# Kernel optimization log

Hardware: AMD Instinct MI355X
Metric: run time of the kernel (lower is better)

## Reference

```python
import jax, jax.numpy as jnp
import numpy as np

B = 64        # number of graph segments
BASE = 384    # mean verts per segment
LMAX = 512    # pad length (counts in [256, 512])
H_DIM = 256
H_DIV = 128   # h_dim // h_dim_div
HEADS = 4
DH = H_DIV // HEADS  # 32


def _counts(seed):
    rng = np.random.default_rng(seed)
    d = rng.integers(-128, 129, B)
    d[1::2] = -d[::2]            # paired so the total is exactly B*BASE
    return (BASE + d).astype(np.int64)


def _pad_indices(counts, L):
    # Gather indices/mask mapping packed ragged tokens -> padded [B, L].
    counts = np.asarray(counts)
    off = np.concatenate([[0], np.cumsum(counts)[:-1]])
    ar = np.arange(L)[None, :]
    mask = ar < counts[:, None]
    idx = np.where(mask, off[:, None] + ar, 0)
    return idx, mask


def setup_inputs() -> dict:
    key = jax.random.key(0)
    ks = jax.random.split(key, 16)
    src_num_verts = _counts(0)
    dst_num_verts = _counts(1)
    total = B * BASE  # 24576 for both src and dst

    def w(k, shape):
        return 0.02 * jax.random.normal(k, shape, jnp.float32)

    return {
        'src_h': jax.random.normal(ks[0], (total, H_DIM), jnp.float32),
        'dst_h': jax.random.normal(ks[1], (total, H_DIM), jnp.float32),
        'src_num_verts': src_num_verts,
        'dst_num_verts': dst_num_verts,
        # 1x1 Conv1d == linear over channels
        'Wq': w(ks[2], (H_DIV, H_DIM)), 'bq': w(ks[3], (H_DIV,)),
        'Wk': w(ks[4], (H_DIV, H_DIM)), 'bk': w(ks[5], (H_DIV,)),
        'Wv': w(ks[6], (H_DIV, H_DIM)), 'bv': w(ks[7], (H_DIV,)),
        'Wm': w(ks[8], (H_DIV, H_DIV)), 'bm': w(ks[9], (H_DIV,)),
        'W1': w(ks[10], (H_DIM, H_DIM + H_DIV)), 'b1': w(ks[11], (H_DIM,)),
        'g1': 1.0 + 0.1 * jax.random.normal(ks[12], (H_DIM,), jnp.float32),
        'be1': w(ks[13], (H_DIM,)),
        'rm1': w(ks[14], (H_DIM,)),
        'rv1': jax.random.uniform(ks[15], (H_DIM,), jnp.float32, 0.5, 1.5),
        'W2': w(jax.random.fold_in(key, 100), (H_DIM, H_DIM)),
        'b2': w(jax.random.fold_in(key, 101), (H_DIM,)),
        'g2': 1.0 + 0.1 * jax.random.normal(jax.random.fold_in(key, 102), (H_DIM,), jnp.float32),
        'be2': w(jax.random.fold_in(key, 103), (H_DIM,)),
        'rm2': w(jax.random.fold_in(key, 104), (H_DIM,)),
        'rv2': jax.random.uniform(jax.random.fold_in(key, 105), (H_DIM,), jnp.float32, 0.5, 1.5),
    }


def _bn(x, g, b, rm, rv):
    # BatchNorm1d in eval mode (running stats)
    return (x - rm) / jnp.sqrt(rv + 1e-5) * g + b


def reference(src_h, dst_h, src_num_verts, dst_num_verts,
              Wq, bq, Wk, bk, Wv, bv, Wm, bm,
              W1, b1, g1, be1, rm1, rv1,
              W2, b2, g2, be2, rm2, rv2):
    didx, dmask = _pad_indices(dst_num_verts, LMAX)
    sidx, smask = _pad_indices(src_num_verts, LMAX)

    # fused projections over all packed tokens (1x1 conv == matmul)
    q = src_h_proj = dst_h @ Wq.T + bq        # [Nd, H_DIV]
    k = src_h @ Wk.T + bk                     # [Ns, H_DIV]
    v = src_h @ Wv.T + bv

    # pad to block-diagonal batched form; channel c = d*HEADS + h per torch view
    qp = q[didx].reshape(B, LMAX, DH, HEADS)
    kp = k[sidx].reshape(B, LMAX, DH, HEADS)
    vp = v[sidx].reshape(B, LMAX, DH, HEADS)

    scores = jnp.einsum('bndh,bmdh->bhnm', qp, kp) / (DH ** 0.5)
    scores = jnp.where(jnp.asarray(smask)[:, None, None, :], scores, -1e9)
    attn = jax.nn.softmax(scores, axis=-1)
    msg = jnp.einsum('bhnm,bmdh->bndh', attn, vp).reshape(B, LMAX, H_DIV)
    msg = msg @ Wm.T + bm                     # merge conv

    bb, ii = np.nonzero(dmask)                # unpad back to packed layout
    h_msg = msg[bb, ii]                       # [Nd, H_DIV]

    x = jnp.concatenate([dst_h, h_msg], axis=-1)
    x = _bn(x @ W1.T + b1, g1, be1, rm1, rv1)
    x = jax.nn.relu(x)
    x = _bn(x @ W2.T + b2, g2, be2, rm2, rv2)
    return dst_h + x
```

## Files before the change

### kernel.cpp

```cpp
#include <hip/hip_runtime.h>
#include <hip/hip_bf16.h>
#include <math.h>

#define B_SEG 64
#define HDIM 256
#define HDIV 128
#define NHEADS 4
#define DH 32
#define QSC 0.17677669529663687f

typedef unsigned short u16;
typedef unsigned int u32;

typedef __attribute__((ext_vector_type(8))) short s8v;
typedef __attribute__((ext_vector_type(4))) float f4v;

__device__ __forceinline__ u16 f2bf(float f) {
    u32 v;
    __builtin_memcpy(&v, &f, 4);
    u32 r = v + 0x7fffu + ((v >> 16) & 1u);
    return (u16)(r >> 16);
}

__device__ __forceinline__ void async_cp16(const u16* g, u16* l) {
    __builtin_amdgcn_global_load_lds(
        (const __attribute__((address_space(1))) u32*)g,
        (__attribute__((address_space(3))) u32*)l, 16, 0, 0);
}

__global__ __launch_bounds__(256) void k_prep(
    const float* __restrict__ Wq, const float* __restrict__ bq,
    const float* __restrict__ Wk, const float* __restrict__ bk,
    const float* __restrict__ Wv, const float* __restrict__ bv,
    const float* __restrict__ Wm, const float* __restrict__ bm,
    const float* __restrict__ W1, const float* __restrict__ b1,
    const float* __restrict__ g1, const float* __restrict__ be1,
    const float* __restrict__ rm1, const float* __restrict__ rv1,
    const float* __restrict__ W2, const float* __restrict__ b2,
    const float* __restrict__ g2, const float* __restrict__ be2,
    const float* __restrict__ rm2, const float* __restrict__ rv2,
    const int* __restrict__ sc_raw, const int* __restrict__ dc_raw,
    const float* __restrict__ src_h, const float* __restrict__ dst_h,
    int* __restrict__ meta,
    u16* __restrict__ pWq, u16* __restrict__ pWkv,
    u16* __restrict__ pW1f, u16* __restrict__ pW2,
    float* __restrict__ bqp, float* __restrict__ bkvp,
    float* __restrict__ sc1, float* __restrict__ sh1,
    float* __restrict__ sc2, float* __restrict__ sh2,
    u16* __restrict__ srcb, u16* __restrict__ dstb, int ntot) {
    if (blockIdx.x < 1028) {
        int idx = blockIdx.x * 256 + threadIdx.x;
        if (idx < 32768) {
            int cp = idx >> 8, k = idx & 255;
            int c = ((cp & 31) << 2) | (cp >> 5);
            pWq[idx] = f2bf(Wq[c * 256 + k]);
        } else if (idx < 98304) {
            int i = idx - 32768;
            int rp = i >> 8, k = i & 255;
            int r = rp & 127;
            int c = ((r & 31) << 2) | (r >> 5);
            float v = (rp < 128) ? Wk[c * 256 + k] : Wv[c * 256 + k];
            pWkv[i] = f2bf(v);
        } else if (idx < 163840) {
            int i = idx - 98304;
            int o = i >> 8, k = i & 255;
            pW1f[o * 384 + k] = f2bf(W1[o * 384 + k]);
        } else if (idx < 196608) {
            int i = idx - 163840;
            int o = i >> 7, cp = i & 127;
            int c = ((cp & 31) << 2) | (cp >> 5);
            float acc = 0.f;
            for (int j = 0; j < 128; j++)
                acc += W1[o * 384 + 256 + j] * Wm[j * 128 + c];
            pW1f[o * 384 + 256 + cp] = f2bf(acc);
        } else if (idx < 262144) {
            int i = idx - 196608;
            pW2[i] = f2bf(W2[i]);
        } else if (idx < 263168) {
            int p = idx - 262144;
            if (p < 128) {
                int c = ((p & 31) << 2) | (p >> 5);
                bqp[p] = bq[c] * QSC;
            } else if (p < 384) {
                int r = p - 128; int rr = r & 127;
                int c = ((rr & 31) << 2) | (rr >> 5);
                bkvp[r] = (r < 128) ? bk[c] : bv[c];
            } else if (p < 640) {
                int o = p - 384;
                float bsum = 0.f;
                for (int j = 0; j < 128; j++)
                    bsum += W1[o * 384 + 256 + j] * bm[j];
                float s = g1[o] * rsqrtf(rv1[o] + 1e-5f);
                sc1[o] = s;
                sh1[o] = (b1[o] + bsum - rm1[o]) * s + be1[o];
            } else if (p < 896) {
                int o = p - 640;
                float s = g2[o] * rsqrtf(rv2[o] + 1e-5f);
                sc2[o] = s;
                sh2[o] = (b2[o] - rm2[o]) * s + be2[o];
            }
        }
    } else if (blockIdx.x == 1028) {
        if (threadIdx.x == 0) {
            bool is64 = (sc_raw[1] == 0);
            int so = 0, dofs = 0;
            for (int i = 0; i < B_SEG; i++) {
                int s = is64 ? sc_raw[2 * i] : sc_raw[i];
                int d = is64 ? dc_raw[2 * i] : dc_raw[i];
                meta[i] = s; meta[64 + i] = d;
                meta[128 + i] = so; meta[192 + i] = dofs;
                so += s; dofs += d;
            }
        }
    } else {
        int i = (blockIdx.x - 1029) * 256 + threadIdx.x;
        int half = ntot * 64;
        const float4* s;
        u16* o;
        int j = i;
        if (i < half) { s = (const float4*)src_h; o = srcb; }
        else { s = (const float4*)dst_h; o = dstb; j = i - half; }
        float4 v = s[j];
        ushort4 u = {f2bf(v.x), f2bf(v.y), f2bf(v.z), f2bf(v.w)};
        ((ushort4*)o)[j] = u;
    }
}

__device__ __forceinline__ void gemm_body(
    const u16* __restrict__ A, int lda,
    const u16* __restrict__ A2, int lda2, int K1,
    const u16* __restrict__ Bw, int K, int m0, int n0,
    const float* __restrict__ scale, const float* __restrict__ shift,
    const float* __restrict__ resid,
    void* __restrict__ Cout, int ldc, int flags,
    u16* Al, u16* Bl) {
    int tid = threadIdx.x;
    int w = tid >> 6, lane = tid & 63;
    int wm = w & 1, wn = w >> 1;
    int l15 = lane & 15, quad = lane >> 4;
    int srow = w * 32 + (lane >> 2);
    int scol = (lane & 3) << 3;
    u16* al0 = Al + w * 1024;
    u16* bl0 = Bl + w * 1024;
    f4v acc[4][4] = {};

    for (int k0 = 0; k0 < K; k0 += 32) {
        const u16* Ag; int aL, acol;
        if (k0 < K1) { Ag = A; aL = lda; acol = k0; }
        else { Ag = A2; aL = lda2; acol = k0 - K1; }
        async_cp16(&Ag[(size_t)(m0 + srow) * aL + acol + scol], al0);
        async_cp16(&Ag[(size_t)(m0 + srow + 16) * aL + acol + scol], al0 + 512);
        async_cp16(&Bw[(size_t)(n0 + srow) * K + k0 + scol], bl0);
        async_cp16(&Bw[(size_t)(n0 + srow + 16) * K + k0 + scol], bl0 + 512);
        __syncthreads();
        s8v af[4], bf[4];
#pragma unroll
        for (int i = 0; i < 4; i++)
            af[i] = *(const s8v*)(&Al[(wm * 64 + i * 16 + l15) * 32 + quad * 8]);
#pragma unroll
        for (int j = 0; j < 4; j++)
            bf[j] = *(const s8v*)(&Bl[(wn * 64 + j * 16 + l15) * 32 + quad * 8]);
#pragma unroll
        for (int i = 0; i < 4; i++)
#pragma unroll
            for (int j = 0; j < 4; j++)
                acc[i][j] = __builtin_amdgcn_mfma_f32_16x16x32_bf16(
                    af[i], bf[j], acc[i][j], 0, 0, 0);
        __syncthreads();
    }
#pragma unroll
    for (int i = 0; i < 4; i++) {
#pragma unroll
        for (int j = 0; j < 4; j++) {
            int n = n0 + wn * 64 + j * 16 + l15;
            float sc = scale ? scale[n] : 1.f;
            float sh = shift ? shift[n] : 0.f;
#pragma unroll
            for (int r = 0; r < 4; r++) {
                int m = m0 + wm * 64 + i * 16 + quad * 4 + r;
                float v = acc[i][j][r];
                if (flags & 4) v *= QSC;
                v = v * sc + sh;
                if (flags & 1) v = fmaxf(v, 0.f);
                if (resid) v += resid[(size_t)m * 256 + n];
                if (flags & 2) ((float*)Cout)[(size_t)m * ldc + n] = v;
                else ((u16*)Cout)[(size_t)m * ldc + n] = f2bf(v);
            }
        }
    }
}

__global__ __launch_bounds__(256) void k_qkv(
    const u16* __restrict__ dstb, const u16* __restrict__ srcb,
    const u16* __restrict__ pWq, const u16* __restrict__ pWkv,
    const float* __restrict__ bqp, const float* __restrict__ bkvp,
    u16* __restrict__ qb, u16* __restrict__ kvb) {
    __shared__ u16 Al[4096];
    __shared__ u16 Bl[4096];
    int m0 = blockIdx.x * 128;
    if (blockIdx.y == 0)
        gemm_body(dstb, 256, dstb, 256, 256, pWq, 256, m0, 0,
                  nullptr, bqp, nullptr, qb, 128, 4, Al, Bl);
    else
        gemm_body(srcb, 256, srcb, 256, 256, pWkv, 256, m0, (blockIdx.y - 1) * 128,
                  nullptr, bkvp, nullptr, kvb, 256, 0, Al, Bl);
}

__global__ __launch_bounds__(256, 4) void k_mlp(
    const u16* __restrict__ dstb, const u16* __restrict__ msgb,
    const u16* __restrict__ pW1f, const u16* __restrict__ pW2,
    const float* __restrict__ sc1, const float* __restrict__ sh1,
    const float* __restrict__ sc2, const float* __restrict__ sh2,
    const float* __restrict__ dst_h, float* __restrict__ out) {
    __shared__ u16 Al[32 * 32];
    __shared__ u16 Bl[256 * 32];
    __shared__ u16 X1[32 * 256];
    int m0 = blockIdx.x * 32;
    int tid = threadIdx.x;
    int w = tid >> 6, lane = tid & 63;
    int l15 = lane & 15, quad = lane >> 4;
    int srow = lane >> 2;
    int scol = (lane & 3) << 3;
    f4v acc[2][4];

#pragma unroll
    for (int i = 0; i < 2; i++)
#pragma unroll
        for (int j = 0; j < 4; j++) acc[i][j] = (f4v){0.f, 0.f, 0.f, 0.f};

    for (int k0 = 0; k0 < 384; k0 += 32) {
        const u16* Ag; int aL, acol;
        if (k0 < 256) { Ag = dstb; aL = 256; acol = k0; }
        else { Ag = msgb; aL = 128; acol = k0 - 256; }
#pragma unroll
        for (int q = 0; q < 4; q++)
            async_cp16(&pW1f[(size_t)(w * 64 + q * 16 + srow) * 384 + k0 + scol],
                       Bl + (w * 64 + q * 16) * 32);
        if (w < 2)
            async_cp16(&Ag[(size_t)(m0 + w * 16 + srow) * aL + acol + scol],
                       Al + w * 16 * 32);
        __syncthreads();
        s8v af[2], bf[4];
#pragma unroll
        for (int i = 0; i < 2; i++)
            af[i] = *(const s8v*)(&Al[(i * 16 + l15) * 32 + quad * 8]);
#pragma unroll
        for (int j = 0; j < 4; j++)
            bf[j] = *(const s8v*)(&Bl[(w * 64 + j * 16 + l15) * 32 + quad * 8]);
#pragma unroll
        for (int i = 0; i < 2; i++)
#pragma unroll
            for (int j = 0; j < 4; j++)
                acc[i][j] = __builtin_amdgcn_mfma_f32_16x16x32_bf16(
                    af[i], bf[j], acc[i][j], 0, 0, 0);
        __syncthreads();
    }
#pragma unroll
    for (int i = 0; i < 2; i++) {
#pragma unroll
        for (int j = 0; j < 4; j++) {
            int n = w * 64 + j * 16 + l15;
            float sc = sc1[n], sh = sh1[n];
#pragma unroll
            for (int r = 0; r < 4; r++) {
                int row = i * 16 + quad * 4 + r;
                float v = fmaxf(acc[i][j][r] * sc + sh, 0.f);
                X1[row * 256 + ((n >> 3) ^ (row & 7)) * 8 + (n & 7)] = f2bf(v);
            }
        }
    }
    __syncthreads();

#pragma unroll
    for (int i = 0; i < 2; i++)
#pragma unroll
        for (int j = 0; j < 4; j++) acc[i][j] = (f4v){0.f, 0.f, 0.f, 0.f};

    for (int k0 = 0; k0 < 256; k0 += 32) {
#pragma unroll
        for (int q = 0; q < 4; q++)
            async_cp16(&pW2[(size_t)(w * 64 + q * 16 + srow) * 256 + k0 + scol],
                       Bl + (w * 64 + q * 16) * 32);
        __syncthreads();
        s8v af[2], bf[4];
#pragma unroll
        for (int i = 0; i < 2; i++) {
            int row = i * 16 + l15;
            af[i] = *(const s8v*)(
                &X1[row * 256 + (((k0 >> 3) + quad) ^ (row & 7)) * 8]);
        }
#pragma unroll
        for (int j = 0; j < 4; j++)
            bf[j] = *(const s8v*)(&Bl[(w * 64 + j * 16 + l15) * 32 + quad * 8]);
#pragma unroll
        for (int i = 0; i < 2; i++)
#pragma unroll
            for (int j = 0; j < 4; j++)
                acc[i][j] = __builtin_amdgcn_mfma_f32_16x16x32_bf16(
                    af[i], bf[j], acc[i][j], 0, 0, 0);
        __syncthreads();
    }
#pragma unroll
    for (int i = 0; i < 2; i++) {
#pragma unroll
        for (int j = 0; j < 4; j++) {
            int n = w * 64 + j * 16 + l15;
            float sc = sc2[n], sh = sh2[n];
#pragma unroll
            for (int r = 0; r < 4; r++) {
                int m = m0 + i * 16 + quad * 4 + r;
                float v = acc[i][j][r] * sc + sh + dst_h[(size_t)m * 256 + n];
                out[(size_t)m * 256 + n] = v;
            }
        }
    }
}

__global__ __launch_bounds__(512, 4) void k_attn(
    const u16* __restrict__ qb, const u16* __restrict__ kvb,
    const int* __restrict__ meta, u16* __restrict__ msgb) {
    extern __shared__ u16 sm[];
    u16* Kl = sm;
    u16* Vl = sm + 16384;
    u16* Pl = sm + 32768;
    int b = blockIdx.x, h = blockIdx.y, z = blockIdx.z;
    int ns = meta[b], nd = meta[64 + b];
    int soff = meta[128 + b], doff = meta[192 + b];
    int tid = threadIdx.x, w = tid >> 6, lane = tid & 63;
    int l15 = lane & 15, quad = lane >> 4;

    {
        int m = tid;
        if (m < ns) {
            const uint4* ks = (const uint4*)&kvb[(size_t)(soff + m) * 256 + h * 32];
#pragma unroll
            for (int s = 0; s < 4; s++)
                *(uint4*)&Kl[m * 32 + (s ^ ((m >> 1) & 3)) * 8] = ks[s];
            uint4 vv[4];
            const uint4* vs =
                (const uint4*)&kvb[(size_t)(soff + m) * 256 + 128 + h * 32];
#pragma unroll
            for (int s = 0; s < 4; s++) vv[s] = vs[s];
            const u16* pv = (const u16*)vv;
#pragma unroll
            for (int d = 0; d < 32; d++)
                Vl[d * 512 + ((m >> 3) ^ (d & 7)) * 8 + (m & 7)] = pv[d];
        } else {
#pragma unroll
            for (int d = 0; d < 32; d++)
                Vl[d * 512 + ((m >> 3) ^ (d & 7)) * 8 + (m & 7)] = 0;
        }
    }
    __syncthreads();

    int nt = (ns + 15) >> 4;
    int nc8 = (ns + 63) >> 6;
    u16* Pw = Pl + w * 1024;

    for (int s0 = (z * 8 + w) * 16; s0 < nd; s0 += 256) {
        int qr = min(s0 + l15, nd - 1);
        s8v aq = *(const s8v*)&qb[(size_t)(doff + qr) * 128 + h * 32 + quad * 8];

        f4v oa0 = {0.f, 0.f, 0.f, 0.f}, oa1 = {0.f, 0.f, 0.f, 0.f};
        float lsum[4] = {0.f, 0.f, 0.f, 0.f};
#pragma unroll
        for (int c = 0; c < 8; c++) {
            if (c < nc8) {
                f4v e4[4];
#pragma unroll
                for (int tt = 0; tt < 4; tt++) {
                    int t = c * 4 + tt;
                    if (t < nt) {
                        int kr = t * 16 + l15;
                        s8v bk = *(const s8v*)&Kl[kr * 32 +
                                                  (quad ^ ((l15 >> 1) & 3)) * 8];
                        f4v s_ = __builtin_amdgcn_mfma_f32_16x16x32_bf16(
                            aq, bk, (f4v){0.f, 0.f, 0.f, 0.f}, 0, 0, 0);
                        bool ok = kr < ns;
#pragma unroll
                        for (int r = 0; r < 4; r++) {
                            float ev = ok ? __expf(s_[r]) : 0.f;
                            e4[tt][r] = ev;
                            lsum[r] += ev;
                        }
                    } else {
#pragma unroll
                        for (int r = 0; r < 4; r++) e4[tt][r] = 0.f;
                    }
                }
#pragma unroll
                for (int tt = 0; tt < 4; tt++)
#pragma unroll
                    for (int r = 0; r < 4; r++) {
                        int row = quad * 4 + r;
                        int slot = tt * 2 + (l15 >> 3);
                        Pw[row * 64 + (slot ^ (row & 7)) * 8 + (l15 & 7)] =
                            f2bf(e4[tt][r]);
                    }
#pragma unroll
                for (int kc = 0; kc < 2; kc++) {
                    s8v ap = *(const s8v*)&Pw[l15 * 64 +
                                              ((kc * 4 + quad) ^ (l15 & 7)) * 8];
                    int vslot = c * 8 + kc * 4 + quad;
                    s8v bv0 = *(const s8v*)&Vl[l15 * 512 +
                                               (vslot ^ (l15 & 7)) * 8];
                    s8v bv1 = *(const s8v*)&Vl[(16 + l15) * 512 +
                                               (vslot ^ (l15 & 7)) * 8];
                    oa0 = __builtin_amdgcn_mfma_f32_16x16x32_bf16(ap, bv0, oa0, 0, 0, 0);
                    oa1 = __builtin_amdgcn_mfma_f32_16x16x32_bf16(ap, bv1, oa1, 0, 0, 0);
                }
            }
        }
        float inv[4];
#pragma unroll
        for (int r = 0; r < 4; r++) {
            float s_ = lsum[r];
#pragma unroll
            for (int x = 1; x < 16; x <<= 1) s_ += __shfl_xor(s_, x, 16);
            inv[r] = 1.f / s_;
        }
#pragma unroll
        for (int r = 0; r < 4; r++) {
            int row = s0 + quad * 4 + r;
            if (row < nd) {
                size_t base = (size_t)(doff + row) * 128 + h * 32;
                msgb[base + l15] = f2bf(oa0[r] * inv[r]);
                msgb[base + 16 + l15] = f2bf(oa1[r] * inv[r]);
            }
        }
    }
}

extern "C" void kernel_launch(void* const* d_in, const int* in_sizes, int n_in,
                              void* d_out, int out_size, void* d_ws, size_t ws_size,
                              hipStream_t stream) {
    const float* src_h = (const float*)d_in[0];
    const float* dst_h = (const float*)d_in[1];
    const int* snv = (const int*)d_in[2];
    const int* dnv = (const int*)d_in[3];
    const float* Wq = (const float*)d_in[4];  const float* bq = (const float*)d_in[5];
    const float* Wk = (const float*)d_in[6];  const float* bk = (const float*)d_in[7];
    const float* Wv = (const float*)d_in[8];  const float* bv = (const float*)d_in[9];
    const float* Wm = (const float*)d_in[10]; const float* bm = (const float*)d_in[11];
    const float* W1 = (const float*)d_in[12]; const float* b1 = (const float*)d_in[13];
    const float* g1 = (const float*)d_in[14]; const float* be1 = (const float*)d_in[15];
    const float* rm1 = (const float*)d_in[16]; const float* rv1 = (const float*)d_in[17];
    const float* W2 = (const float*)d_in[18]; const float* b2 = (const float*)d_in[19];
    const float* g2 = (const float*)d_in[20]; const float* be2 = (const float*)d_in[21];
    const float* rm2 = (const float*)d_in[22]; const float* rv2 = (const float*)d_in[23];

    int ntot = out_size / HDIM;
    int mt = ntot / 128;

    char* ws = (char*)d_ws;
    int* meta = (int*)ws;
    float* bqp = (float*)(ws + 4096);
    float* bkvp = (float*)(ws + 4608);
    float* sc1 = (float*)(ws + 6144);
    float* sh1 = (float*)(ws + 7168);
    float* sc2 = (float*)(ws + 8192);
    float* sh2 = (float*)(ws + 9216);
    u16* pWq = (u16*)(ws + 16384);
    u16* pWkv = (u16*)(ws + 81920);
    u16* pW1f = (u16*)(ws + 212992);
    u16* pW2 = (u16*)(ws + 409600);
    u16* srcb = (u16*)(ws + 1048576);
    u16* dstb = (u16*)(ws + 13631488);
    u16* msgb = (u16*)(ws + 26214400);

    u16* qb = (u16*)d_out;
    u16* kvb = qb + (size_t)ntot * 128;

    hipFuncSetAttribute((const void*)k_attn,
                        hipFuncAttributeMaxDynamicSharedMemorySize, 81920);

    k_prep<<<dim3(1029 + ntot / 2), dim3(256), 0, stream>>>(
        Wq, bq, Wk, bk, Wv, bv, Wm, bm, W1, b1, g1, be1, rm1, rv1,
        W2, b2, g2, be2, rm2, rv2, snv, dnv, src_h, dst_h, meta,
        pWq, pWkv, pW1f, pW2, bqp, bkvp, sc1, sh1, sc2, sh2,
        srcb, dstb, ntot);
    k_qkv<<<dim3(mt, 3), dim3(256), 0, stream>>>(
        dstb, srcb, pWq, pWkv, bqp, bkvp, qb, kvb);
    k_attn<<<dim3(B_SEG, NHEADS, 2), dim3(512), 81920, stream>>>(
        qb, kvb, meta, msgb);
    k_mlp<<<dim3(ntot / 32), dim3(256), 0, stream>>>(
        dstb, msgb, pW1f, pW2, sc1, sh1, sc2, sh2, dst_h, (float*)d_out);
}
```

Before: 207.2 us.

## Compute transposed scores in attention and pass P via shuffles instead of LDS

The attention kernel now computes S^T by swapping the MFMA operands (K as A, Q as B). The bf16-packed exp values are then redistributed into the A-operand layout for the PV MFMA with cross-lane shuffles, replacing the per-wave LDS staging buffer for P. This drops the P scratch region, shrinking dynamic shared memory from 80KB to 64KB. It also swaps the fully unrolled 8-chunk loop for a 32-key runtime loop and changes the row-sum reduction. The aim is to cut LDS writes/reads and allow more blocks per CU, at the cost of many shuffle instructions per chunk.

```diff
diff --git a/kernel.cpp b/kernel.cpp
--- a/kernel.cpp
+++ b/kernel.cpp
@@ -322,7 +322,6 @@
     extern __shared__ u16 sm[];
     u16* Kl = sm;
     u16* Vl = sm + 16384;
-    u16* Pl = sm + 32768;
     int b = blockIdx.x, h = blockIdx.y, z = blockIdx.z;
     int ns = meta[b], nd = meta[64 + b];
     int soff = meta[128 + b], doff = meta[192 + b];
@@ -353,79 +352,72 @@
     }
     __syncthreads();
 
-    int nt = (ns + 15) >> 4;
-    int nc8 = (ns + 63) >> 6;
-    u16* Pw = Pl + w * 1024;
+    int nc32 = (ns + 31) >> 5;
+    int srcA = (quad & 1) * 32 + l15;
+    int srcB = srcA + 16;
+    int ksw = (quad ^ ((l15 >> 1) & 3)) * 8;
 
     for (int s0 = (z * 8 + w) * 16; s0 < nd; s0 += 256) {
         int qr = min(s0 + l15, nd - 1);
         s8v aq = *(const s8v*)&qb[(size_t)(doff + qr) * 128 + h * 32 + quad * 8];
 
         f4v oa0 = {0.f, 0.f, 0.f, 0.f}, oa1 = {0.f, 0.f, 0.f, 0.f};
-        float lsum[4] = {0.f, 0.f, 0.f, 0.f};
-#pragma unroll
-        for (int c = 0; c < 8; c++) {
-            if (c < nc8) {
-                f4v e4[4];
-#pragma unroll
-                for (int tt = 0; tt < 4; tt++) {
-                    int t = c * 4 + tt;
-                    if (t < nt) {
-                        int kr = t * 16 + l15;
-                        s8v bk = *(const s8v*)&Kl[kr * 32 +
-                                                  (quad ^ ((l15 >> 1) & 3)) * 8];
-                        f4v s_ = __builtin_amdgcn_mfma_f32_16x16x32_bf16(
-                            aq, bk, (f4v){0.f, 0.f, 0.f, 0.f}, 0, 0, 0);
-                        bool ok = kr < ns;
-#pragma unroll
-                        for (int r = 0; r < 4; r++) {
-                            float ev = ok ? __expf(s_[r]) : 0.f;
-                            e4[tt][r] = ev;
-                            lsum[r] += ev;
-                        }
-                    } else {
-#pragma unroll
-                        for (int r = 0; r < 4; r++) e4[tt][r] = 0.f;
-                    }
-                }
-#pragma unroll
-                for (int tt = 0; tt < 4; tt++)
-#pragma unroll
-                    for (int r = 0; r < 4; r++) {
-                        int row = quad * 4 + r;
-                        int slot = tt * 2 + (l15 >> 3);
-                        Pw[row * 64 + (slot ^ (row & 7)) * 8 + (l15 & 7)] =
-                            f2bf(e4[tt][r]);
-                    }
-#pragma unroll
-                for (int kc = 0; kc < 2; kc++) {
-                    s8v ap = *(const s8v*)&Pw[l15 * 64 +
-                                              ((kc * 4 + quad) ^ (l15 & 7)) * 8];
-                    int vslot = c * 8 + kc * 4 + quad;
-                    s8v bv0 = *(const s8v*)&Vl[l15 * 512 +
-                                               (vslot ^ (l15 & 7)) * 8];
-                    s8v bv1 = *(const s8v*)&Vl[(16 + l15) * 512 +
-                                               (vslot ^ (l15 & 7)) * 8];
-                    oa0 = __builtin_amdgcn_mfma_f32_16x16x32_bf16(ap, bv0, oa0, 0, 0, 0);
-                    oa1 = __builtin_amdgcn_mfma_f32_16x16x32_bf16(ap, bv1, oa1, 0, 0, 0);
-                }
-            }
-        }
-        float inv[4];
-#pragma unroll
-        for (int r = 0; r < 4; r++) {
-            float s_ = lsum[r];
-#pragma unroll
-            for (int x = 1; x < 16; x <<= 1) s_ += __shfl_xor(s_, x, 16);
-            inv[r] = 1.f / s_;
-        }
+        float lsum = 0.f;
+#pragma unroll 2
+        for (int c = 0; c < nc32; c++) {
+            int kr0 = c * 32 + l15;
+            s8v bk0 = *(const s8v*)&Kl[kr0 * 32 + ksw];
+            s8v bk1 = *(const s8v*)&Kl[(kr0 + 16) * 32 + ksw];
+            f4v sa = __builtin_amdgcn_mfma_f32_16x16x32_bf16(
+                bk0, aq, (f4v){0.f, 0.f, 0.f, 0.f}, 0, 0, 0);
+            f4v sb = __builtin_amdgcn_mfma_f32_16x16x32_bf16(
+                bk1, aq, (f4v){0.f, 0.f, 0.f, 0.f}, 0, 0, 0);
+            int kb = c * 32 + quad * 4;
+            float e0[4], e1[4];
+#pragma unroll
+            for (int r = 0; r < 4; r++) {
+                float va = (kb + r < ns) ? __expf(sa[r]) : 0.f;
+                float vb = (kb + 16 + r < ns) ? __expf(sb[r]) : 0.f;
+                e0[r] = va; e1[r] = vb;
+                lsum += va + vb;
+            }
+            u32 p01_0 = (u32)f2bf(e0[0]) | ((u32)f2bf(e0[1]) << 16);
+            u32 p23_0 = (u32)f2bf(e0[2]) | ((u32)f2bf(e0[3]) << 16);
+            u32 p01_1 = (u32)f2bf(e1[0]) | ((u32)f2bf(e1[1]) << 16);
+            u32 p23_1 = (u32)f2bf(e1[2]) | ((u32)f2bf(e1[3]) << 16);
+            int t0a = __shfl((int)p01_0, srcA, 64);
+            int t0b = __shfl((int)p23_0, srcA, 64);
+            int t0c = __shfl((int)p01_0, srcB, 64);
+            int t0d = __shfl((int)p23_0, srcB, 64);
+            int t1a = __shfl((int)p01_1, srcA, 64);
+            int t1b = __shfl((int)p23_1, srcA, 64);
+            int t1c = __shfl((int)p01_1, srcB, 64);
+            int t1d = __shfl((int)p23_1, srcB, 64);
+            union { s8v v; int u[4]; } pa;
+            bool lo = quad < 2;
+            pa.u[0] = lo ? t0a : t1a;
+            pa.u[1] = lo ? t0b : t1b;
+            pa.u[2] = lo ? t0c : t1c;
+            pa.u[3] = lo ? t0d : t1d;
+            int vs = ((c * 4 + quad) ^ (l15 & 7)) * 8;
+            s8v bv0 = *(const s8v*)&Vl[l15 * 512 + vs];
+            s8v bv1 = *(const s8v*)&Vl[(16 + l15) * 512 + vs];
+            oa0 = __builtin_amdgcn_mfma_f32_16x16x32_bf16(pa.v, bv0, oa0, 0, 0, 0);
+            oa1 = __builtin_amdgcn_mfma_f32_16x16x32_bf16(pa.v, bv1, oa1, 0, 0, 0);
+        }
+        lsum += __shfl_xor(lsum, 16, 64);
+        lsum += __shfl_xor(lsum, 32, 64);
+        float inv = 1.f / lsum;
+        float iq[4];
+#pragma unroll
+        for (int r = 0; r < 4; r++) iq[r] = __shfl(inv, quad * 4 + r, 64);
 #pragma unroll
         for (int r = 0; r < 4; r++) {
             int row = s0 + quad * 4 + r;
             if (row < nd) {
                 size_t base = (size_t)(doff + row) * 128 + h * 32;
-                msgb[base + l15] = f2bf(oa0[r] * inv[r]);
-                msgb[base + 16 + l15] = f2bf(oa1[r] * inv[r]);
+                msgb[base + l15] = f2bf(oa0[r] * iq[r]);
+                msgb[base + 16 + l15] = f2bf(oa1[r] * iq[r]);
             }
         }
     }
@@ -472,7 +464,7 @@
     u16* kvb = qb + (size_t)ntot * 128;
 
     hipFuncSetAttribute((const void*)k_attn,
-                        hipFuncAttributeMaxDynamicSharedMemorySize, 81920);
+                        hipFuncAttributeMaxDynamicSharedMemorySize, 65536);
 
     k_prep<<<dim3(1029 + ntot / 2), dim3(256), 0, stream>>>(
         Wq, bq, Wk, bk, Wv, bv, Wm, bm, W1, b1, g1, be1, rm1, rv1,
@@ -481,7 +473,7 @@
         srcb, dstb, ntot);
     k_qkv<<<dim3(mt, 3), dim3(256), 0, stream>>>(
         dstb, srcb, pWq, pWkv, bqp, bkvp, qb, kvb);
-    k_attn<<<dim3(B_SEG, NHEADS, 2), dim3(512), 81920, stream>>>(
+    k_attn<<<dim3(B_SEG, NHEADS, 2), dim3(512), 65536, stream>>>(
         qb, kvb, meta, msgb);
     k_mlp<<<dim3(ntot / 32), dim3(256), 0, stream>>>(
         dstb, msgb, pW1f, pW2, sc1, sh1, sc2, sh2, dst_h, (float*)d_out);
```

Result: no change. 204.7 us (-1.2%).
